# Kernel optimization log

Measured on AMD Instinct MI355X. Metric: run time of the kernel, lower is better.

The kernel has to match this reference:

```python
import jax, jax.numpy as jnp
import numpy as np

B, F, HU, HC = 8192, 100, 128, 512


def _lin(key, din, dout, bias=True, scale=0.02):
    k1, k2 = jax.random.split(key)
    w = jax.random.normal(k1, (din, dout), jnp.float32) * scale
    if bias:
        b = jax.random.normal(k2, (dout,), jnp.float32) * scale
        return w, b
    return (w,)


def setup_inputs() -> dict:
    key = jax.random.key(0)
    ks = jax.random.split(key, 24)
    d = {}
    d['feature_list'] = jax.random.normal(ks[0], (B, F), jnp.float32)
    d['is_treat'] = jax.random.uniform(ks[1], (B,), jnp.float32)
    d['emb'] = jax.random.normal(ks[2], (F, HU), jnp.float32) * 0.02
    d['t_w'], d['t_b'] = _lin(ks[3], 1, HU)
    d['qw'], d['qb'] = _lin(ks[4], HU, HU)
    d['kw'], d['kb'] = _lin(ks[5], HU, HU)
    d['vw'], d['vb'] = _lin(ks[6], HU, HU)
    (d['a1w'],) = _lin(ks[7], HU, HU, bias=False)
    d['a2w'], d['a2b'] = _lin(ks[8], HU, HU)
    (d['a3w'],) = _lin(ks[9], HU, 1, bias=False)
    d['c1w'], d['c1b'] = _lin(ks[10], F * HU, HC)
    d['c2w'], d['c2b'] = _lin(ks[11], HC, HC)
    d['c3w'], d['c3b'] = _lin(ks[12], HC, HC // 2)
    d['c4w'], d['c4b'] = _lin(ks[13], HC // 2, HC // 4)
    d['c5w'], d['c5b'] = _lin(ks[14], HC // 4, HC // 8)
    d['clw'], d['clb'] = _lin(ks[15], HC // 8, 1)
    d['ctw'], d['ctb'] = _lin(ks[16], HC // 8, 1)
    d['u1w'], d['u1b'] = _lin(ks[17], HU, HU)
    d['u2w'], d['u2b'] = _lin(ks[18], HU, HU // 2)
    d['u3w'], d['u3b'] = _lin(ks[19], HU // 2, HU // 4)
    d['u4w'], d['u4b'] = _lin(ks[20], HU // 4, HU // 8)
    d['tlw'], d['tlb'] = _lin(ks[21], HU // 8, 1)
    d['utw'], d['utb'] = _lin(ks[22], HU // 8, 1)
    return d


def reference(feature_list, is_treat, emb, t_w, t_b, qw, qb, kw, kb, vw, vb,
              a1w, a2w, a2b, a3w, c1w, c1b, c2w, c2b, c3w, c3b, c4w, c4b,
              c5w, c5b, clw, clb, ctw, ctb, u1w, u1b, u2w, u2b, u3w, u3b,
              u4w, u4b, tlw, tlb, utw, utb):
    elu = jax.nn.elu
    sig = jax.nn.sigmoid
    b, f = feature_list.shape
    h = emb.shape[1]
    # per-feature embedding: [B, F, H]
    x_rep = feature_list[:, :, None] * emb[None, :, :]
    # normalize over the feature axis (dim=1), as in torch.linalg.norm(dim=1)
    nx = x_rep / jnp.linalg.norm(x_rep, axis=1, keepdims=True)
    # self-attention with sigmoid-then-softmax scores
    Q = nx @ qw + qb
    K = nx @ kw + kb
    V = nx @ vw + vb
    scores = jnp.einsum('bfh,bgh->bfg', Q, K) / (h ** 0.5)
    attn_w = jax.nn.softmax(sig(scores), axis=-1)
    xx = jnp.einsum('bfg,bgh->bfh', attn_w, V).reshape(b, f * h)
    # control net tower
    c = elu(xx @ c1w + c1b)
    c = elu(c @ c2w + c2b)
    c = elu(c @ c3w + c3b)
    c = elu(c @ c4w + c4b)
    c = elu(c @ c5w + c5b)  # is_self=True
    c_logit = c @ clw + clb
    c_tau = c @ ctw + ctb
    c_prob = sig(c_logit)
    # treatment representation: Linear(1, hu) on ones -> [B, H]
    t_rep = jnp.ones((b, 1), feature_list.dtype) @ t_w.reshape(1, h) + t_b
    # interaction attention (vectorized over features)
    att = jax.nn.relu(sig(t_rep @ a1w)[:, None, :] + sig(x_rep @ a2w + a2b))
    att = (att @ a3w)[..., 0]  # [B, F]
    attn = jax.nn.softmax(att, axis=1)
    xt = jnp.einsum('bf,bfh->bh', attn, x_rep)
    # uplift net tower
    u = elu(xt @ u1w + u1b)
    u = elu(u @ u2w + u2b)
    u = elu(u @ u3w + u3b)
    u = elu(u @ u4w + u4b)  # is_self=True
    t_logit = u @ tlw + tlb
    u_tau = u @ utw + utb
    t_prob = sig(t_logit)
    return (c_logit, c_prob, c_tau, t_logit, t_prob, u_tau)
```

## Files before the change

### kernel.cpp

```cpp
#include <hip/hip_runtime.h>
#include <hip/hip_bf16.h>

typedef __bf16 bf16;
typedef __bf16 bf16x8 __attribute__((ext_vector_type(8)));
typedef __bf16 bf16x4 __attribute__((ext_vector_type(4)));
typedef float f32x4 __attribute__((ext_vector_type(4)));
typedef unsigned u32x4 __attribute__((ext_vector_type(4)));

#define DEVI static __device__ __forceinline__

DEVI float sigmoidf_(float x){ return 1.0f/(1.0f+__expf(-x)); }
DEVI float eluf_(float x){ return x>0.f ? x : (__expf(x)-1.f); }
DEVI f32x4 mfma16(bf16x8 a, bf16x8 b, f32x4 c){ return __builtin_amdgcn_mfma_f32_16x16x32_bf16(a,b,c,0,0,0); }
DEVI f32x4 mfma8(long a, long b, f32x4 c){ return __builtin_amdgcn_mfma_f32_16x16x32_fp8_fp8(a,b,c,0,0,0); }
DEVI unsigned pack2_(float a, float b){
    union { bf16 v[2]; unsigned u; } t; t.v[0]=(bf16)a; t.v[1]=(bf16)b; return t.u;
}
DEVI unsigned long long pack4_(float a, float b, float c, float d){
    union { bf16 v[4]; unsigned long long u; } t;
    t.v[0]=(bf16)a; t.v[1]=(bf16)b; t.v[2]=(bf16)c; t.v[3]=(bf16)d; return t.u;
}
DEVI unsigned cvtfp8x4_(float a, float b, float c, float d){
    int v = __builtin_amdgcn_cvt_pk_fp8_f32(a, b, 0, false);
    v = __builtin_amdgcn_cvt_pk_fp8_f32(c, d, v, true);
    return (unsigned)v;
}

#define B_ 8192
#define F_ 100
#define FP 112
#define H_ 128
#define KC_ 12800
#define SPLIT_ 4
#define FP8SC 16.0f

#define SWZ(r,bc) ((bc) ^ (((r)&7)<<4))

DEVI void dotrans_(float (*t)[33], const float* in, bf16* out, int R, int C, int bx, int by, int tid){
    int c0 = bx*32, r0 = by*32;
    int tc = tid & 31, tr = tid >> 5;
    #pragma unroll
    for (int i=0;i<4;i++){
        int r = tr + i*8;
        t[r][tc] = in[(size_t)(r0+r)*C + c0 + tc];
    }
    __syncthreads();
    #pragma unroll
    for (int i=0;i<4;i++){
        int ro = tr + i*8;
        out[(size_t)(c0+ro)*R + r0 + tc] = (bf16)t[tc][ro];
    }
}

__global__ void k_prep_all(const float* __restrict__ qw, const float* __restrict__ qb,
                           const float* __restrict__ kw, const float* __restrict__ kb,
                           const float* __restrict__ tw, const float* __restrict__ tb,
                           const float* __restrict__ a1w, const float* __restrict__ vw,
                           const float* __restrict__ a2w, const float* __restrict__ c2w,
                           const float* __restrict__ c3w,
                           bf16* __restrict__ mextT, float* __restrict__ sigt, float* __restrict__ cconst,
                           bf16* __restrict__ wvT, bf16* __restrict__ wa2t,
                           bf16* __restrict__ c2wt, bf16* __restrict__ c3wt){
    __shared__ float t[32][33];
    const float rsc = 0.08838834764831845f;
    int blk = blockIdx.x, tid = threadIdx.x;
    if (blk < 9){
        #pragma unroll 1
        for (int e=0; e<8; ++e){
            int idx = e*256 + tid;
            int n = blk*16 + (idx>>7), h = idx&127;
            float acc = 0.f;
            if (n < 128){
                for (int d=0; d<128; ++d) acc += qw[h*128+d]*kw[n*128+d];
            } else if (n == 128){
                for (int d=0; d<128; ++d) acc += qw[h*128+d]*kb[d];
            } else if (n == 129){
                for (int d=0; d<128; ++d) acc += kw[h*128+d]*qb[d];
            }
            mextT[n*128+h] = (bf16)(acc*rsc);
        }
    } else if (blk == 9){
        if (tid < 128){
            float acc = 0.f;
            for (int h=0; h<128; ++h) acc += (tw[h]+tb[h]) * a1w[h*128+tid];
            sigt[tid] = sigmoidf_(acc);
        } else if (tid == 128){
            float acc = 0.f;
            for (int d=0; d<128; ++d) acc += qb[d]*kb[d];
            cconst[0] = acc*rsc;
        }
    } else if (blk < 26){
        int i = blk-10; dotrans_(t, vw, wvT, 128,128, i&3, i>>2, tid);
    } else if (blk < 42){
        int i = blk-26; dotrans_(t, a2w, wa2t, 128,128, i&3, i>>2, tid);
    } else if (blk < 298){
        int i = blk-42; dotrans_(t, c2w, c2wt, 512,512, i&15, i>>4, tid);
    } else {
        int i = blk-298; dotrans_(t, c3w, c3wt, 512,256, i&7, i>>3, tid);
    }
}

DEVI int kappa_(int k){
    int f = k>>7, h = k&127;
    if (f < 96)
        return (((f>>4)<<3) | (h>>4))*256 + ((f&15)>>2)*64 + (h&15)*4 + (f&3);
    else
        return 12288 + (h>>4)*64 + (h&15)*4 + (f&3);
}

__global__ __launch_bounds__(256,2) void k_gk(
    const float* __restrict__ c1w, unsigned char* __restrict__ c1wtk8,
    const float* __restrict__ feat, const float* __restrict__ emb,
    const bf16* __restrict__ wa2t, const float* __restrict__ a2b,
    const float* __restrict__ a3w, const float* __restrict__ sigt,
    float* __restrict__ attg)
{
    __shared__ char A[37888];
    int blk = blockIdx.x, tid = threadIdx.x;
    if (blk < 6400){
        float (*t)[33] = (float(*)[33])A;
        const int C = 512;
        int c0 = (blk&15)*32, r0 = (blk>>4)*32;
        int tc = tid & 31, tr = tid >> 5;
        #pragma unroll
        for (int i=0;i<4;i++){
            int r = tr + i*8;
            t[r][tc] = c1w[(size_t)(r0+r)*C + c0 + tc];
        }
        __syncthreads();
        #pragma unroll
        for (int i=0;i<4;i++){
            int ro = tr + i*8;
            float x = t[tc][ro]*FP8SC;
            int v = __builtin_amdgcn_cvt_pk_fp8_f32(x, x, 0, false);
            c1wtk8[(size_t)(c0+ro)*KC_ + kappa_(r0+tc)] = (unsigned char)v;
        }
        return;
    }
    bf16 (*sAt)[72] = (bf16(*)[72])A;
    bf16 (*sBt)[72] = (bf16(*)[72])(A + 18432);
    float (*sRed)[128] = (float(*)[128])(A + 36864);
    int w=tid>>6, lane=tid&63, l15=lane&15, l4=lane>>4;
    int m0 = (blk-6400)*128;
    int wr = w>>1, wc = w&1;
    f32x4 acc[4][4];
    #pragma unroll
    for(int mi=0;mi<4;mi++)
        #pragma unroll
        for(int ni=0;ni<4;ni++) acc[mi][ni] = (f32x4){0.f,0.f,0.f,0.f};

    #pragma unroll 1
    for (int k0=0; k0<128; k0+=64){
        __syncthreads();
        #pragma unroll
        for (int t4=0; t4<4; t4++){
            int t = tid + t4*256;
            int row=t>>3, col=(t&7)*8;
            int gr = m0+row;
            int bb = gr/112, ff = gr - bb*112;
            bf16x8 o;
            if (ff < F_){
                float fv = feat[(size_t)bb*F_ + ff];
                const float* ep = emb + ff*H_ + k0 + col;
                f32x4 e0 = *(const f32x4*)ep;
                f32x4 e1 = *(const f32x4*)(ep+4);
                o[0]=(bf16)(fv*e0[0]); o[1]=(bf16)(fv*e0[1]); o[2]=(bf16)(fv*e0[2]); o[3]=(bf16)(fv*e0[3]);
                o[4]=(bf16)(fv*e1[0]); o[5]=(bf16)(fv*e1[1]); o[6]=(bf16)(fv*e1[2]); o[7]=(bf16)(fv*e1[3]);
            } else {
                #pragma unroll
                for (int e=0;e<8;e++) o[e]=(bf16)0.f;
            }
            *(bf16x8*)&sAt[row][col] = o;
            *(bf16x8*)&sBt[row][col] = *(const bf16x8*)(wa2t + row*H_ + k0 + col);
        }
        __syncthreads();
        #pragma unroll
        for(int ks=0;ks<2;ks++){
            bf16x8 af[4], bfr[4];
            #pragma unroll
            for(int mi=0;mi<4;mi++) af[mi] = *(const bf16x8*)&sAt[wr*64+mi*16+l15][ks*32+l4*8];
            #pragma unroll
            for(int ni=0;ni<4;ni++) bfr[ni] = *(const bf16x8*)&sBt[wc*64+ni*16+l15][ks*32+l4*8];
            #pragma unroll
            for(int mi=0;mi<4;mi++)
                #pragma unroll
                for(int ni=0;ni<4;ni++)
                    acc[mi][ni] = mfma16(af[mi], bfr[ni], acc[mi][ni]);
        }
    }
    float sg[4], ab[4], a3[4];
    #pragma unroll
    for (int ni=0;ni<4;ni++){
        int n = wc*64 + ni*16 + l15;
        sg[ni]=sigt[n]; ab[ni]=a2b[n]; a3[ni]=a3w[n];
    }
    #pragma unroll
    for (int mi=0;mi<4;mi++){
        float sj[4] = {0.f,0.f,0.f,0.f};
        #pragma unroll
        for (int ni=0;ni<4;ni++){
            #pragma unroll
            for (int j=0;j<4;j++){
                float u = sigmoidf_(acc[mi][ni][j] + ab[ni]);
                float t = sg[ni] + u;
                t = t>0.f ? t : 0.f;
                sj[j] += t*a3[ni];
            }
        }
        #pragma unroll
        for (int j=0;j<4;j++){
            float v = sj[j];
            #pragma unroll
            for (int m=1;m<16;m<<=1) v += __shfl_xor(v,m,16);
            sj[j]=v;
        }
        if (l15==0){
            #pragma unroll
            for (int j=0;j<4;j++) sRed[wc][wr*64+mi*16+l4*4+j] = sj[j];
        }
    }
    __syncthreads();
    if (tid < 128) attg[(size_t)m0 + tid] = sRed[0][tid] + sRed[1][tid];
}

__global__ __launch_bounds__(512,2) void k_attn2(
    const float* __restrict__ feat, const float* __restrict__ emb,
    const bf16* __restrict__ mextT, const bf16* __restrict__ wvT,
    const float* __restrict__ vb, const float* __restrict__ cconst,
    const float* __restrict__ attg,
    unsigned char* __restrict__ xxb, bf16* __restrict__ xtb)
{
    __shared__ char L[81792];
    char* Lm = L;
    char* Ln = L + 32768;
    float* sFeat  = (float*)(L+61440);
    float* normP  = (float*)(L+62336);
    float* sAw    = (float*)(L+77568);
    float* sNorm  = (float*)(L+79872);
    float* sAlpha = (float*)(L+80384);
    float* sBeta  = (float*)(L+80832);
    float* sInv   = (float*)(L+81280);

    int b = blockIdx.x;
    int tid = threadIdx.x, w = tid>>6, lane = tid&63;
    int l15 = lane&15, l4 = lane>>4;
    bf16 (*sP)[72] = (bf16(*)[72])(L + 61440 + w*2304);

    bf16x8 awv[4];
    #pragma unroll
    for (int kc=0;kc<4;kc++)
        awv[kc] = *(const bf16x8*)(wvT + (w*16+l15)*H_ + kc*32 + l4*8);
    float vbr = vb[w*16+l15];

    #pragma unroll 2
    for (int v = tid; v < 128*16; v += 512){
        int n = v >> 4, cg = (v & 15) * 8;
        *(u32x4*)(Lm + n*256 + SWZ(n, cg*2)) = *(const u32x4*)(mextT + n*128 + cg);
    }
    if (tid < FP) sFeat[tid] = (tid<F_) ? feat[(size_t)b*F_+tid] : 0.f;
    if (w==0){
        const float* ag = attg + (size_t)b*FP;
        float a0 = (lane<F_)? ag[lane] : -1e30f;
        float a1 = (lane+64<F_)? ag[lane+64] : -1e30f;
        float m = fmaxf(a0,a1);
        #pragma unroll
        for(int s=1;s<64;s<<=1) m = fmaxf(m, __shfl_xor(m,s,64));
        float e0 = (lane<F_)? __expf(a0-m):0.f;
        float e1 = (lane+64<F_)? __expf(a1-m):0.f;
        float s = e0+e1;
        #pragma unroll
        for(int t=1;t<64;t<<=1) s += __shfl_xor(s,t,64);
        float inv = 1.f/s;
        if (lane<FP) sAw[lane] = e0*inv;
        if (lane+64<FP) sAw[lane+64] = e1*inv;
    }
    __syncthreads();

    int hp = (tid&63)*2, gg = tid>>6;
    {
        float fa0=0.f, fa1=0.f;
        #pragma unroll 4
        for (int it=0; it<13; ++it){
            int f = gg + 8*it;
            if (f < F_){
                float2 e2 = *(const float2*)(emb + f*H_ + hp);
                float v0 = sFeat[f]*e2.x, v1 = sFeat[f]*e2.y;
                fa0 += v0*v0; fa1 += v1*v1;
            }
        }
        *(float2*)(normP + gg*128 + hp) = make_float2(fa0, fa1);
    }
    __syncthreads();
    if (tid < 128){
        float s = 0.f;
        #pragma unroll
        for (int g2=0; g2<8; ++g2) s += normP[g2*128 + tid];
        sNorm[tid] = sqrtf(s);
    }
    __syncthreads();

    {
        float rn0 = __builtin_amdgcn_rcpf(sNorm[hp]);
        float rn1 = __builtin_amdgcn_rcpf(sNorm[hp+1]);
        #pragma unroll 4
        for (int it=0; it<13; ++it){
            int f = gg + 8*it;
            if (f < F_){
                float2 e2 = *(const float2*)(emb + f*H_ + hp);
                *(unsigned*)(Ln + f*256 + SWZ(f, hp*2)) = pack2_(sFeat[f]*e2.x*rn0, sFeat[f]*e2.y*rn1);
            }
        }
        for (int z=tid; z<768; z+=512){
            int f = 100 + (z>>6), hz = (z&63)*2;
            *(unsigned*)(Ln + f*256 + SWZ(f, hz*2)) = 0u;
        }
    }
    __syncthreads();

    int mt = w;

    if (mt < 7){
        bf16x8 bfr8[4];
        #pragma unroll
        for (int kc=0;kc<4;kc++)
            bfr8[kc] = *(const bf16x8*)(mextT + (128+(l15&1))*H_ + kc*32 + l4*8);
        f32x4 acc = {0.f,0.f,0.f,0.f};
        #pragma unroll
        for (int kc=0;kc<4;kc++){
            bf16x8 a = *(const bf16x8*)(Ln + (mt*16+l15)*256 + SWZ(mt*16+l15, (kc*32+l4*8)*2));
            acc = mfma16(a, bfr8[kc], acc);
        }
        if (l15==0){
            #pragma unroll
            for (int j=0;j<4;j++) sAlpha[mt*16+l4*4+j] = acc[j];
        }
        if (l15==1){
            #pragma unroll
            for (int j=0;j<4;j++) sBeta[mt*16+l4*4+j] = acc[j];
        }
    }
    __syncthreads();

    const float cc = cconst[0];
    unsigned long long uexB[3];
    if (mt < 7){
        bf16x8 afxi[4];
        #pragma unroll
        for (int kc=0;kc<4;kc++)
            afxi[kc] = *(const bf16x8*)(Ln + (mt*16+l15)*256 + SWZ(mt*16+l15, (kc*32+l4*8)*2));
        f32x4 sc[7];
        #pragma unroll
        for (int gt=0; gt<7; gt++) sc[gt] = (f32x4){0.f,0.f,0.f,0.f};
        #pragma unroll 1
        for (int p=0; p<2; p++){
            #pragma unroll 2
            for (int nt4=0; nt4<4; nt4++){
                int nt = p*4 + nt4;
                bf16x8 bw[4];
                #pragma unroll
                for (int kc=0;kc<4;kc++)
                    bw[kc] = *(const bf16x8*)(Lm + (nt*16+l15)*256 + SWZ(nt*16+l15, (kc*32+l4*8)*2));
                f32x4 d = {0.f,0.f,0.f,0.f};
                #pragma unroll
                for (int kc=0;kc<4;kc++) d = mfma16(bw[kc], afxi[kc], d);
                *(unsigned long long*)(&sP[l15][nt4*16 + l4*4]) = pack4_(d[0],d[1],d[2],d[3]);
            }
            bf16x8 afs0 = *(const bf16x8*)&sP[l15][l4*8];
            bf16x8 afs1 = *(const bf16x8*)&sP[l15][32+l4*8];
            #pragma unroll
            for (int gt=0; gt<7; gt++){
                int r = gt*16+l15;
                bf16x8 b0 = *(const bf16x8*)(Ln + r*256 + SWZ(r, (p*64 + l4*8)*2));
                bf16x8 b1 = *(const bf16x8*)(Ln + r*256 + SWZ(r, (p*64 + 32 + l4*8)*2));
                sc[gt] = mfma16(b0, afs0, sc[gt]);
                sc[gt] = mfma16(b1, afs1, sc[gt]);
            }
        }
        float aj = sAlpha[mt*16+l15];
        float rs = 0.f;
        #pragma unroll
        for (int gt=0; gt<7; gt++){
            f32x4 bt4 = *(const f32x4*)&sBeta[gt*16+l4*4];
            float e[4];
            #pragma unroll
            for (int j=0;j<4;j++){
                int g = gt*16 + l4*4 + j;
                float val = sc[gt][j] + aj + bt4[j] + cc;
                e[j] = (g<F_) ? __expf(sigmoidf_(val)) : 0.f;
                rs += e[j];
            }
            if (gt < 4)
                *(unsigned long long*)(&sP[l15][gt*16 + l4*4]) = pack4_(e[0],e[1],e[2],e[3]);
            else
                uexB[gt-4] = pack4_(e[0],e[1],e[2],e[3]);
        }
        rs += __shfl_xor(rs, 16, 64);
        rs += __shfl_xor(rs, 32, 64);
        if (l4 == 0) sInv[w*16 + l15] = 1.f/rs;
    } else {
        int h = lane;
        float a0=0.f, a1=0.f;
        #pragma unroll 4
        for (int f=0; f<F_; ++f){
            float awf = sAw[f];
            a0 += awf * (float)*(const bf16*)(Ln + f*256 + SWZ(f, h*2));
            a1 += awf * (float)*(const bf16*)(Ln + f*256 + SWZ(f, (h+64)*2));
        }
        xtb[(size_t)b*H_ + h]      = (bf16)(a0 * sNorm[h]);
        xtb[(size_t)b*H_ + h + 64] = (bf16)(a1 * sNorm[h+64]);
    }

    unsigned long long vpku[7];
    #pragma unroll
    for (int gt=0; gt<7; gt++){
        f32x4 acc = {0.f,0.f,0.f,0.f};
        #pragma unroll
        for (int kc=0;kc<4;kc++){
            int r = gt*16+l15;
            bf16x8 a = *(const bf16x8*)(Ln + r*256 + SWZ(r, (kc*32+l4*8)*2));
            acc = mfma16(a, awv[kc], acc);
        }
        vpku[gt] = pack4_(acc[0]+vbr, acc[1]+vbr, acc[2]+vbr, acc[3]+vbr);
    }
    __syncthreads();

    {
        int hrow = w*16 + l15;
        #pragma unroll
        for (int gt=0; gt<7; gt++)
            *(unsigned long long*)(Lm + hrow*256 + SWZ(hrow, gt*32 + l4*8)) = vpku[gt];
    }
    __syncthreads();

    if (mt < 7){
        bf16x8 ap0 = *(const bf16x8*)&sP[l15][l4*8];
        bf16x8 ap1 = *(const bf16x8*)&sP[l15][32+l4*8];
        f32x4 acc8[8];
        #pragma unroll
        for (int ht=0;ht<8;ht++) acc8[ht] = (f32x4){0.f,0.f,0.f,0.f};
        #pragma unroll
        for (int ht=0; ht<8; ht++){
            int r = ht*16+l15;
            bf16x8 bv0 = *(const bf16x8*)(Lm + r*256 + SWZ(r, (l4*8)*2));
            bf16x8 bv1 = *(const bf16x8*)(Lm + r*256 + SWZ(r, (32+l4*8)*2));
            acc8[ht] = mfma16(ap0, bv0, acc8[ht]);
            acc8[ht] = mfma16(ap1, bv1, acc8[ht]);
        }
        #pragma unroll
        for (int gt=4; gt<7; gt++)
            *(unsigned long long*)(&sP[l15][(gt-4)*16 + l4*4]) = uexB[gt-4];
        *(unsigned long long*)(&sP[l15][48 + l4*4]) = 0ull;
        bf16x8 ap2 = *(const bf16x8*)&sP[l15][l4*8];
        bf16x8 ap3 = *(const bf16x8*)&sP[l15][32+l4*8];
        #pragma unroll
        for (int ht=0; ht<8; ht++){
            int r = ht*16+l15;
            int c2 = 64+l4*8;
            int c3 = 96+l4*8;  if (c3 >= 112) c3 = 96;
            bf16x8 bv2 = *(const bf16x8*)(Lm + r*256 + SWZ(r, c2*2));
            bf16x8 bv3 = *(const bf16x8*)(Lm + r*256 + SWZ(r, c3*2));
            acc8[ht] = mfma16(ap2, bv2, acc8[ht]);
            acc8[ht] = mfma16(ap3, bv3, acc8[ht]);
        }
        float fs[4];
        #pragma unroll
        for (int j=0;j<4;j++) fs[j] = sInv[w*16 + l4*4 + j] * FP8SC;
        #pragma unroll
        for (int ht=0; ht<8; ht++){
            unsigned u = cvtfp8x4_(acc8[ht][0]*fs[0], acc8[ht][1]*fs[1], acc8[ht][2]*fs[2], acc8[ht][3]*fs[3]);
            if (mt < 6){
                *(unsigned*)(xxb + (size_t)b*KC_ + (mt*8+ht)*256 + lane*4) = u;
            } else if (l4 == 0){
                *(unsigned*)(xxb + (size_t)b*KC_ + 12288 + ht*64 + l15*4) = u;
            }
        }
    }
}

__global__ __launch_bounds__(512,2) void k_gemm_fp8(const unsigned char* __restrict__ A,
        const unsigned char* __restrict__ Bt, bf16* __restrict__ part, int M, int N, int K, int KS)
{
    __shared__ unsigned char sA[128][144];
    __shared__ unsigned char sB[256][144];
    int tid=threadIdx.x, w=tid>>6, lane=tid&63, l15=lane&15, l4=lane>>4;
    int m0 = blockIdx.y*128, n0 = blockIdx.x*256;
    int kbeg = blockIdx.z*KS, kend = kbeg + KS;
    int wr = w>>2, wc = w&3;
    f32x4 acc[4][4];
    #pragma unroll
    for(int mi=0;mi<4;mi++)
        #pragma unroll
        for(int ni=0;ni<4;ni++) acc[mi][ni] = (f32x4){0.f,0.f,0.f,0.f};

    for (int k0=kbeg; k0<kend; k0+=128){
        __syncthreads();
        #pragma unroll
        for (int t2=0;t2<2;t2++){
            int t = tid + t2*512;
            int row=t>>3, col=(t&7)*16;
            *(u32x4*)&sA[row][col] = *(const u32x4*)(A + (size_t)(m0+row)*K + k0 + col);
        }
        #pragma unroll
        for (int t4=0;t4<4;t4++){
            int t = tid + t4*512;
            int row=t>>3, col=(t&7)*16;
            *(u32x4*)&sB[row][col] = *(const u32x4*)(Bt + (size_t)(n0+row)*K + k0 + col);
        }
        __syncthreads();
        #pragma unroll
        for(int ks=0;ks<4;ks++){
            long af[4], bfr[4];
            #pragma unroll
            for(int mi=0;mi<4;mi++) af[mi] = *(const long*)&sA[wr*64+mi*16+l15][ks*32+l4*8];
            #pragma unroll
            for(int ni=0;ni<4;ni++) bfr[ni] = *(const long*)&sB[wc*64+ni*16+l15][ks*32+l4*8];
            #pragma unroll
            for(int mi=0;mi<4;mi++)
                #pragma unroll
                for(int ni=0;ni<4;ni++)
                    acc[mi][ni] = mfma8(af[mi], bfr[ni], acc[mi][ni]);
        }
    }
    bf16* pz = part + (size_t)blockIdx.z*M*N;
    #pragma unroll
    for(int mi=0;mi<4;mi++)
        #pragma unroll
        for(int ni=0;ni<4;ni++){
            int col = n0 + wc*64 + ni*16 + l15;
            #pragma unroll
            for(int j=0;j<4;j++){
                int row = m0 + wr*64 + mi*16 + l4*4 + j;
                pz[(size_t)row*N + col] = (bf16)acc[mi][ni][j];
            }
        }
}

__global__ void k_c1fin(const bf16* __restrict__ part, const float* __restrict__ bias,
                        bf16* __restrict__ out){
    const size_t MN = (size_t)B_*512;
    size_t e0 = ((size_t)blockIdx.x*256 + threadIdx.x)*4;
    bf16x4 p0 = *(const bf16x4*)(part + e0);
    bf16x4 p1 = *(const bf16x4*)(part + MN + e0);
    bf16x4 p2 = *(const bf16x4*)(part + 2*MN + e0);
    bf16x4 p3 = *(const bf16x4*)(part + 3*MN + e0);
    f32x4 bb = *(const f32x4*)(bias + (e0 & 511));
    const float ds = 1.0f/(FP8SC*FP8SC);
    float s0 = ((float)p0[0]+(float)p1[0]+(float)p2[0]+(float)p3[0])*ds + bb[0];
    float s1 = ((float)p0[1]+(float)p1[1]+(float)p2[1]+(float)p3[1])*ds + bb[1];
    float s2 = ((float)p0[2]+(float)p1[2]+(float)p2[2]+(float)p3[2])*ds + bb[2];
    float s3 = ((float)p0[3]+(float)p1[3]+(float)p2[3]+(float)p3[3])*ds + bb[3];
    unsigned long long u = pack4_(eluf_(s0), eluf_(s1), eluf_(s2), eluf_(s3));
    *(unsigned long long*)(out + e0) = u;
}

template<int BN, bool ELU>
__global__ __launch_bounds__(256,2) void k_gemm(const bf16* __restrict__ A, const bf16* __restrict__ Bt,
        const float* __restrict__ bias, bf16* __restrict__ out, int M, int N, int K)
{
    __shared__ bf16 sAt[128][72];
    __shared__ bf16 sBt[BN][72];
    int tid=threadIdx.x, w=tid>>6, lane=tid&63, l15=lane&15, l4=lane>>4;
    int m0 = blockIdx.y*128, n0 = blockIdx.x*BN;
    constexpr int MI = (BN==128)?4:2;
    constexpr int NI = (BN==128)?4:BN/16;
    int wr = (BN==128)? (w>>1) : w;
    int wc = (BN==128)? (w&1) : 0;
    f32x4 acc[MI][NI];
    #pragma unroll
    for(int mi=0;mi<MI;mi++)
        #pragma unroll
        for(int ni=0;ni<NI;ni++) acc[mi][ni] = (f32x4){0.f,0.f,0.f,0.f};

    for (int k0=0; k0<K; k0+=64){
        __syncthreads();
        for (int t=tid; t<128*8; t+=256){
            int row=t>>3, col=(t&7)*8;
            *(bf16x8*)&sAt[row][col] = *(const bf16x8*)(A + (size_t)(m0+row)*K + k0 + col);
        }
        for (int t=tid; t<BN*8; t+=256){
            int row=t>>3, col=(t&7)*8;
            *(bf16x8*)&sBt[row][col] = *(const bf16x8*)(Bt + (size_t)(n0+row)*K + k0 + col);
        }
        __syncthreads();
        #pragma unroll
        for(int ks=0;ks<2;ks++){
            bf16x8 af[MI], bfr[NI];
            #pragma unroll
            for(int mi=0;mi<MI;mi++) af[mi] = *(const bf16x8*)&sAt[wr*(MI*16)+mi*16+l15][ks*32+l4*8];
            #pragma unroll
            for(int ni=0;ni<NI;ni++) bfr[ni] = *(const bf16x8*)&sBt[wc*64+ni*16+l15][ks*32+l4*8];
            #pragma unroll
            for(int mi=0;mi<MI;mi++)
                #pragma unroll
                for(int ni=0;ni<NI;ni++)
                    acc[mi][ni] = mfma16(af[mi], bfr[ni], acc[mi][ni]);
        }
    }
    #pragma unroll
    for(int mi=0;mi<MI;mi++)
        #pragma unroll
        for(int ni=0;ni<NI;ni++){
            int col = n0 + wc*64 + ni*16 + l15;
            float bc = bias[col];
            #pragma unroll
            for(int j=0;j<4;j++){
                int row = m0 + wr*(MI*16) + mi*16 + l4*4 + j;
                float v = acc[mi][ni][j] + bc;
                if (ELU) v = eluf_(v);
                out[(size_t)row*N + col] = (bf16)v;
            }
        }
}

__global__ __launch_bounds__(256,2) void k_tails(const bf16* __restrict__ c3o,
    const float* __restrict__ c4w, const float* __restrict__ c4b,
    const float* __restrict__ c5w, const float* __restrict__ c5b,
    const float* __restrict__ clw, const float* __restrict__ clb,
    const float* __restrict__ ctw, const float* __restrict__ ctb,
    const bf16* __restrict__ xtb,
    const float* __restrict__ u1w, const float* __restrict__ u1b,
    const float* __restrict__ u2w, const float* __restrict__ u2b,
    const float* __restrict__ u3w, const float* __restrict__ u3b,
    const float* __restrict__ u4w, const float* __restrict__ u4b,
    const float* __restrict__ tlw, const float* __restrict__ tlb,
    const float* __restrict__ utw, const float* __restrict__ utb, float* __restrict__ outp)
{
    __shared__ char A[58880];
    int tid = threadIdx.x, blk = blockIdx.x;
    int r0 = (blk>>1)*32;
    if ((blk & 1) == 0){
        float (*sA)[260] = (float(*)[260])A;
        float (*sB)[132] = (float(*)[132])(A + 33280);
        float (*sC)[68]  = (float(*)[68])(A + 50176);
        for (int v=tid; v<32*64; v+=256){
            int r=v>>6, c=(v&63)*4;
            bf16x4 x = *(const bf16x4*)(c3o + (size_t)(r0+r)*256 + c);
            sA[r][c]=(float)x[0]; sA[r][c+1]=(float)x[1]; sA[r][c+2]=(float)x[2]; sA[r][c+3]=(float)x[3];
        }
        __syncthreads();
        {
            int j = tid&127, rb = tid>>7;
            float acc[16];
            #pragma unroll
            for (int i=0;i<16;i++) acc[i]=c4b[j];
            #pragma unroll 4
            for (int h=0;h<256;h++){
                float wv = c4w[h*128+j];
                #pragma unroll
                for (int i=0;i<16;i++) acc[i] += sA[2*i+rb][h]*wv;
            }
            #pragma unroll
            for (int i=0;i<16;i++) sB[2*i+rb][j] = eluf_(acc[i]);
        }
        __syncthreads();
        {
            int j = tid&63, rb = tid>>6;
            float acc[8];
            #pragma unroll
            for (int i=0;i<8;i++) acc[i]=c5b[j];
            #pragma unroll 4
            for (int h=0;h<128;h++){
                float wv = c5w[h*64+j];
                #pragma unroll
                for (int i=0;i<8;i++) acc[i] += sB[4*i+rb][h]*wv;
            }
            #pragma unroll
            for (int i=0;i<8;i++) sC[4*i+rb][j] = eluf_(acc[i]);
        }
        __syncthreads();
        if (tid < 32){
            float r1 = clb[0], r2 = ctb[0];
            #pragma unroll 8
            for (int k=0;k<64;k++){ float v = sC[tid][k]; r1 += v*clw[k]; r2 += v*ctw[k]; }
            int row = r0 + tid;
            outp[row] = r1;
            outp[B_ + row] = sigmoidf_(r1);
            outp[(size_t)2*B_ + row] = r2;
        }
    } else {
        float (*sA)[132] = (float(*)[132])A;
        float (*sB)[132] = (float(*)[132])(A + 16896);
        float (*sC)[68]  = (float(*)[68])(A + 33792);
        float (*sD)[36]  = (float(*)[36])(A + 42496);
        float (*sE)[20]  = (float(*)[20])(A + 47104);
        for (int v=tid; v<32*32; v+=256){
            int r=v>>5, c=(v&31)*4;
            bf16x4 x = *(const bf16x4*)(xtb + (size_t)(r0+r)*128 + c);
            sA[r][c]=(float)x[0]; sA[r][c+1]=(float)x[1]; sA[r][c+2]=(float)x[2]; sA[r][c+3]=(float)x[3];
        }
        __syncthreads();
        {
            int j = tid&127, rb = tid>>7;
            float acc[16];
            #pragma unroll
            for (int i=0;i<16;i++) acc[i]=u1b[j];
            #pragma unroll 4
            for (int h=0;h<128;h++){
                float wv = u1w[h*128+j];
                #pragma unroll
                for (int i=0;i<16;i++) acc[i] += sA[2*i+rb][h]*wv;
            }
            #pragma unroll
            for (int i=0;i<16;i++) sB[2*i+rb][j] = eluf_(acc[i]);
        }
        __syncthreads();
        {
            int j = tid&63, rb = tid>>6;
            float acc[8];
            #pragma unroll
            for (int i=0;i<8;i++) acc[i]=u2b[j];
            #pragma unroll 4
            for (int h=0;h<128;h++){
                float wv = u2w[h*64+j];
                #pragma unroll
                for (int i=0;i<8;i++) acc[i] += sB[4*i+rb][h]*wv;
            }
            #pragma unroll
            for (int i=0;i<8;i++) sC[4*i+rb][j] = eluf_(acc[i]);
        }
        __syncthreads();
        {
            int j = tid&31, rb = tid>>5;
            float acc[4];
            #pragma unroll
            for (int i=0;i<4;i++) acc[i]=u3b[j];
            #pragma unroll 4
            for (int h=0;h<64;h++){
                float wv = u3w[h*32+j];
                #pragma unroll
                for (int i=0;i<4;i++) acc[i] += sC[8*i+rb][h]*wv;
            }
            #pragma unroll
            for (int i=0;i<4;i++) sD[8*i+rb][j] = eluf_(acc[i]);
        }
        __syncthreads();
        {
            int j = tid&15, rb = tid>>4;
            float acc0=u4b[j], acc1=u4b[j];
            #pragma unroll 4
            for (int h=0;h<32;h++){
                float wv = u4w[h*16+j];
                acc0 += sD[rb][h]*wv;
                acc1 += sD[16+rb][h]*wv;
            }
            sE[rb][j] = eluf_(acc0);
            sE[16+rb][j] = eluf_(acc1);
        }
        __syncthreads();
        if (tid < 32){
            float r1 = tlb[0], r2 = utb[0];
            #pragma unroll
            for (int k=0;k<16;k++){ float v = sE[tid][k]; r1 += v*tlw[k]; r2 += v*utw[k]; }
            int row = r0 + tid;
            outp[(size_t)3*B_ + row] = r1;
            outp[(size_t)4*B_ + row] = sigmoidf_(r1);
            outp[(size_t)5*B_ + row] = r2;
        }
    }
}

extern "C" void kernel_launch(void* const* d_in, const int* in_sizes, int n_in,
                              void* d_out, int out_size, void* d_ws, size_t ws_size,
                              hipStream_t stream) {
    const float* feat=(const float*)d_in[0];
    const float* emb =(const float*)d_in[2];
    const float* t_w =(const float*)d_in[3]; const float* t_b=(const float*)d_in[4];
    const float* qw  =(const float*)d_in[5]; const float* qb =(const float*)d_in[6];
    const float* kw  =(const float*)d_in[7]; const float* kb =(const float*)d_in[8];
    const float* vw  =(const float*)d_in[9]; const float* vb =(const float*)d_in[10];
    const float* a1w =(const float*)d_in[11];
    const float* a2w =(const float*)d_in[12]; const float* a2b=(const float*)d_in[13];
    const float* a3w =(const float*)d_in[14];
    const float* c1w =(const float*)d_in[15]; const float* c1b=(const float*)d_in[16];
    const float* c2w =(const float*)d_in[17]; const float* c2b=(const float*)d_in[18];
    const float* c3w =(const float*)d_in[19]; const float* c3b=(const float*)d_in[20];
    const float* c4w =(const float*)d_in[21]; const float* c4b=(const float*)d_in[22];
    const float* c5w =(const float*)d_in[23]; const float* c5b=(const float*)d_in[24];
    const float* clw =(const float*)d_in[25]; const float* clb=(const float*)d_in[26];
    const float* ctw =(const float*)d_in[27]; const float* ctb=(const float*)d_in[28];
    const float* u1w =(const float*)d_in[29]; const float* u1b=(const float*)d_in[30];
    const float* u2w =(const float*)d_in[31]; const float* u2b=(const float*)d_in[32];
    const float* u3w =(const float*)d_in[33]; const float* u3b=(const float*)d_in[34];
    const float* u4w =(const float*)d_in[35]; const float* u4b=(const float*)d_in[36];
    const float* tlw =(const float*)d_in[37]; const float* tlb=(const float*)d_in[38];
    const float* utw =(const float*)d_in[39]; const float* utb=(const float*)d_in[40];
    float* outp = (float*)d_out;

    char* ws = (char*)d_ws;
    size_t off = 0;
    auto alloc = [&](size_t bytes)->char*{ char* p = ws + off; off += (bytes + 255) & ~(size_t)255; return p; };
    unsigned char* xxb = (unsigned char*)alloc((size_t)B_*KC_);
    bf16* part   = (bf16*)alloc((size_t)SPLIT_*B_*512*2);
    float* attg  = (float*)alloc((size_t)B_*FP*4);
    bf16* xtb    = (bf16*)alloc((size_t)B_*128*2);
    bf16* cbuf1  = (bf16*)alloc((size_t)B_*512*2);
    bf16* mextT  = (bf16*)alloc(144*128*2);
    bf16* wvT    = (bf16*)alloc(128*128*2);
    bf16* wa2t   = (bf16*)alloc(128*128*2);
    unsigned char* c1wtk8 = (unsigned char*)alloc((size_t)512*KC_);
    bf16* c2wt   = (bf16*)alloc((size_t)512*512*2);
    bf16* c3wt   = (bf16*)alloc((size_t)512*256*2);
    float* sigt  = (float*)alloc(128*4);
    float* cconst= (float*)alloc(4);
    bf16* cbuf2 = (bf16*)(xxb);
    bf16* cbuf3 = (bf16*)(xxb + (16u<<20));
    (void)ws_size; (void)in_sizes; (void)n_in; (void)out_size;

    k_prep_all<<<426,256,0,stream>>>(qw,qb,kw,kb,t_w,t_b,a1w, vw, a2w, c2w, c3w,
                                     mextT, sigt, cconst, wvT, wa2t, c2wt, c3wt);

    k_gk<<<13568,256,0,stream>>>(c1w, c1wtk8, feat, emb, wa2t, a2b, a3w, sigt, attg);

    k_attn2<<<B_,512,0,stream>>>(feat,emb,mextT,wvT,vb,cconst,attg, xxb, xtb);

    k_gemm_fp8<<<dim3(2,64,SPLIT_),512,0,stream>>>(xxb, c1wtk8, part, B_,512,KC_, KC_/SPLIT_);
    k_c1fin<<<4096,256,0,stream>>>(part, c1b, cbuf1);

    k_gemm<128,true><<<dim3(4,64),256,0,stream>>>(cbuf1, c2wt, c2b, cbuf2, B_,512,512);
    k_gemm<64,true><<<dim3(4,64),256,0,stream>>>(cbuf2, c3wt, c3b, cbuf3, B_,256,512);

    k_tails<<<512,256,0,stream>>>(cbuf3,c4w,c4b,c5w,c5b,clw,clb,ctw,ctb,
                                  xtb,u1w,u1b,u2w,u2b,u3w,u3b,u4w,u4b,tlw,tlb,utw,utb,outp);
}
```

Measured before the change: 632.2 us.

## Use direct global-to-LDS loads with pre-swizzled FP8 operands in split-K GEMM

The FP8 GEMM now loads A and B tiles straight into LDS with global_load_lds 16-byte transfers, so data no longer passes through registers. The padded 144-byte rows are replaced by dense 128-byte rows. To avoid LDS bank conflicts without padding, the producers of xxb and the transposed c1 weights write their K index XOR-swizzled by row, and the GEMM reads with the matching XOR. This cuts register pressure and the LDS store instructions in the main loop. It ties the layout of the producer kernels to the GEMM's tile shape.

```diff
diff --git a/kernel.cpp b/kernel.cpp
--- a/kernel.cpp
+++ b/kernel.cpp
@@ -24,6 +24,10 @@
     int v = __builtin_amdgcn_cvt_pk_fp8_f32(a, b, 0, false);
     v = __builtin_amdgcn_cvt_pk_fp8_f32(c, d, v, true);
     return (unsigned)v;
+}
+DEVI void gld16_(const void* g, void* l){
+    __builtin_amdgcn_global_load_lds((const __attribute__((address_space(1))) void*)g,
+                                     (__attribute__((address_space(3))) void*)l, 16, 0, 0);
 }
 
 #define B_ 8192
@@ -35,6 +39,7 @@
 #define FP8SC 16.0f
 
 #define SWZ(r,bc) ((bc) ^ (((r)&7)<<4))
+DEVI int swzk_(int row, int k){ return (k & ~127) | ((k & 127) ^ ((row&7)<<4)); }
 
 DEVI void dotrans_(float (*t)[33], const float* in, bf16* out, int R, int C, int bx, int by, int tid){
     int c0 = bx*32, r0 = by*32;
@@ -133,7 +138,8 @@
             int ro = tr + i*8;
             float x = t[tc][ro]*FP8SC;
             int v = __builtin_amdgcn_cvt_pk_fp8_f32(x, x, 0, false);
-            c1wtk8[(size_t)(c0+ro)*KC_ + kappa_(r0+tc)] = (unsigned char)v;
+            int n = c0+ro;
+            c1wtk8[(size_t)n*KC_ + swzk_(n, kappa_(r0+tc))] = (unsigned char)v;
         }
         return;
     }
@@ -469,9 +475,9 @@
         for (int ht=0; ht<8; ht++){
             unsigned u = cvtfp8x4_(acc8[ht][0]*fs[0], acc8[ht][1]*fs[1], acc8[ht][2]*fs[2], acc8[ht][3]*fs[3]);
             if (mt < 6){
-                *(unsigned*)(xxb + (size_t)b*KC_ + (mt*8+ht)*256 + lane*4) = u;
+                *(unsigned*)(xxb + (size_t)b*KC_ + swzk_(b, (mt*8+ht)*256 + lane*4)) = u;
             } else if (l4 == 0){
-                *(unsigned*)(xxb + (size_t)b*KC_ + 12288 + ht*64 + l15*4) = u;
+                *(unsigned*)(xxb + (size_t)b*KC_ + swzk_(b, 12288 + ht*64 + l15*4)) = u;
             }
         }
     }
@@ -480,40 +486,37 @@
 __global__ __launch_bounds__(512,2) void k_gemm_fp8(const unsigned char* __restrict__ A,
         const unsigned char* __restrict__ Bt, bf16* __restrict__ part, int M, int N, int K, int KS)
 {
-    __shared__ unsigned char sA[128][144];
-    __shared__ unsigned char sB[256][144];
+    __shared__ unsigned char S[49152];
     int tid=threadIdx.x, w=tid>>6, lane=tid&63, l15=lane&15, l4=lane>>4;
     int m0 = blockIdx.y*128, n0 = blockIdx.x*256;
     int kbeg = blockIdx.z*KS, kend = kbeg + KS;
     int wr = w>>2, wc = w&3;
+    int offW = w*1024 + lane*16;
+    int rS = offW >> 7, cS = offW & 127;
     f32x4 acc[4][4];
     #pragma unroll
     for(int mi=0;mi<4;mi++)
         #pragma unroll
         for(int ni=0;ni<4;ni++) acc[mi][ni] = (f32x4){0.f,0.f,0.f,0.f};
 
+    int sx = (l15&7)<<4;
+
     for (int k0=kbeg; k0<kend; k0+=128){
         __syncthreads();
-        #pragma unroll
-        for (int t2=0;t2<2;t2++){
-            int t = tid + t2*512;
-            int row=t>>3, col=(t&7)*16;
-            *(u32x4*)&sA[row][col] = *(const u32x4*)(A + (size_t)(m0+row)*K + k0 + col);
-        }
-        #pragma unroll
-        for (int t4=0;t4<4;t4++){
-            int t = tid + t4*512;
-            int row=t>>3, col=(t&7)*16;
-            *(u32x4*)&sB[row][col] = *(const u32x4*)(Bt + (size_t)(n0+row)*K + k0 + col);
-        }
+        gld16_(A + (size_t)(m0 + rS     )*K + k0 + cS, S + offW);
+        gld16_(A + (size_t)(m0 + rS + 64)*K + k0 + cS, S + offW + 8192);
+        #pragma unroll
+        for (int q=0;q<4;q++)
+            gld16_(Bt + (size_t)(n0 + q*64 + rS)*K + k0 + cS, S + 16384 + q*8192 + offW);
         __syncthreads();
         #pragma unroll
         for(int ks=0;ks<4;ks++){
+            int co = (ks*32 + l4*8) ^ sx;
             long af[4], bfr[4];
             #pragma unroll
-            for(int mi=0;mi<4;mi++) af[mi] = *(const long*)&sA[wr*64+mi*16+l15][ks*32+l4*8];
-            #pragma unroll
-            for(int ni=0;ni<4;ni++) bfr[ni] = *(const long*)&sB[wc*64+ni*16+l15][ks*32+l4*8];
+            for(int mi=0;mi<4;mi++) af[mi] = *(const long*)(S + (wr*64+mi*16+l15)*128 + co);
+            #pragma unroll
+            for(int ni=0;ni<4;ni++) bfr[ni] = *(const long*)(S + 16384 + (wc*64+ni*16+l15)*128 + co);
             #pragma unroll
             for(int mi=0;mi<4;mi++)
                 #pragma unroll
```

New measurement: 620.8 us. About the same (-1.8%).
